# Kernel tuning notes

Hardware: AMD Instinct MI355X
Metric: run time of the kernel (lower is better)

## Reference

```python
import jax, jax.numpy as jnp
import numpy as np

N = 50000   # nodes
E = 800000  # edges (before self-loops)


def _gcn_conv(X, W, b, src, dst, dinv, n):
    # PyG GCNConv: out[i] = sum_j norm_ij * (X W)[j] + b, norm_ij = d_i^-1/2 d_j^-1/2
    h = X @ W                                   # [N, d_out]
    norm = dinv[src] * dinv[dst]                # [E+N]
    msg = h[src] * norm[:, None]                # gather + scale
    return jax.ops.segment_sum(msg, dst, num_segments=n) + b


def setup_inputs() -> dict:
    key = jax.random.key(0)
    k1, k2, k3, k4 = jax.random.split(key, 4)
    X = jax.random.normal(k1, (N, 128), dtype=jnp.float32)
    edge_index = jax.random.randint(k2, (2, E), 0, N, dtype=jnp.int64)
    W1 = jax.random.normal(k3, (128, 128), dtype=jnp.float32) * (1.0 / np.sqrt(128))
    b1 = jnp.zeros((128,), jnp.float32)
    W2 = jax.random.normal(k4, (128, 64), dtype=jnp.float32) * (1.0 / np.sqrt(128))
    b2 = jnp.zeros((64,), jnp.float32)
    return {"X": X, "edge_index": edge_index, "W1": W1, "b1": b1, "W2": W2, "b2": b2}


def reference(X, edge_index, W1, b1, W2, b2):
    n = X.shape[0]
    loops = jnp.arange(n, dtype=edge_index.dtype)
    src = jnp.concatenate([edge_index[0], loops])   # A + I
    dst = jnp.concatenate([edge_index[1], loops])
    deg = jax.ops.segment_sum(jnp.ones(src.shape[0], X.dtype), dst, num_segments=n)
    dinv = jnp.where(deg > 0, jax.lax.rsqrt(deg), 0.0)

    h = _gcn_conv(X, W1, b1, src, dst, dinv, n)                     # gcn1
    h = jax.nn.relu(_gcn_conv(h, W1, b1, src, dst, dinv, n))        # gcn1 again (as in source), relu
    # dropout: eval mode (identity)
    logits = _gcn_conv(h, W2, b2, src, dst, dinv, n)                # gcn2
    return jax.nn.log_softmax(logits, axis=1)
```

## Files before the change

kernel.cpp:

```cpp
#include <hip/hip_runtime.h>
#include <hip/hip_fp16.h>
#include <type_traits>

typedef _Float16 f16x8 __attribute__((ext_vector_type(8)));
typedef float    f32x4 __attribute__((ext_vector_type(4)));

__device__ inline unsigned int pack2(float a, float b) {
    __half2 h = __floats2half2_rn(a, b);
    return *(unsigned int*)&h;
}
__device__ inline float2 unpack2(unsigned int u) {
    __half2 h = *(__half2*)&u;
    return __half22float2(h);
}

#define MAXB 8192


__global__ void zero_kernel(int* __restrict__ p, int len) {
    int i = blockIdx.x * blockDim.x + threadIdx.x;
    if (i < len) p[i] = 0;
}

__global__ __launch_bounds__(256) void bucket_scatter_kernel(
    const int* __restrict__ src, const int* __restrict__ dst, int E, int nbuck,
    int* __restrict__ bcursor, unsigned int* __restrict__ staging) {
    __shared__ int hist[256];
    __shared__ int base[256];
    const int t = threadIdx.x;
    const int chunk = (E + gridDim.x - 1) / gridDim.x;
    const int e0 = blockIdx.x * chunk;
    const int e1 = min(E, e0 + chunk);
    for (int i = t; i < nbuck; i += 256) hist[i] = 0;
    __syncthreads();
    for (int e = e0 + t; e < e1; e += 256)
        atomicAdd(&hist[((unsigned)dst[e]) >> 8], 1);
    __syncthreads();
    for (int i = t; i < nbuck; i += 256) {
        int c = hist[i];
        base[i] = (c > 0) ? atomicAdd(&bcursor[i], c) : 0;
        hist[i] = 0;
    }
    __syncthreads();
    for (int e = e0 + t; e < e1; e += 256) {
        int d = dst[e];
        int b = ((unsigned)d) >> 8;
        int off = atomicAdd(&hist[b], 1);
        staging[(size_t)b * MAXB + base[b] + off] =
            (unsigned)src[e] | ((unsigned)(d & 255) << 16);
    }
}

__global__ __launch_bounds__(256) void bucket_hist_kernel(
    const unsigned int* __restrict__ staging, const int* __restrict__ bcursor,
    int n, int* __restrict__ counts) {
    __shared__ int hist[256];
    const int b = blockIdx.x, t = threadIdx.x;
    hist[t] = 0;
    __syncthreads();
    const int cnt = bcursor[b];
    const unsigned int* rec = staging + (size_t)b * MAXB;
    for (int i = t; i < cnt; i += 256) atomicAdd(&hist[(rec[i] >> 16) & 255], 1);
    __syncthreads();
    int node = (b << 8) + t;
    if (node < n) counts[node] = hist[t];
}

__global__ void dinv_kernel(const int* __restrict__ counts, float* __restrict__ dinv, int n) {
    int i = blockIdx.x * blockDim.x + threadIdx.x;
    if (i < n) dinv[i] = rsqrtf(1.0f + (float)counts[i]);
}


__global__ __launch_bounds__(256) void block_sum_kernel(const int* __restrict__ counts, int n,
                                                        int* __restrict__ blocksums) {
    __shared__ int s[256];
    int t = threadIdx.x;
    int i = blockIdx.x * 256 + t;
    s[t] = (i < n) ? counts[i] : 0;
    __syncthreads();
#pragma unroll
    for (int off = 128; off >= 1; off >>= 1) {
        if (t < off) s[t] += s[t + off];
        __syncthreads();
    }
    if (t == 0) blocksums[blockIdx.x] = s[0];
}

__global__ __launch_bounds__(256) void scan_blocksums_kernel(int* __restrict__ blocksums, int nb) {
    __shared__ int s[256];
    int t = threadIdx.x;
    int v = (t < nb) ? blocksums[t] : 0;
    s[t] = v;
    __syncthreads();
    for (int off = 1; off < 256; off <<= 1) {
        int u = (t >= off) ? s[t - off] : 0;
        __syncthreads();
        s[t] += u;
        __syncthreads();
    }
    if (t < nb) blocksums[t] = s[t] - v;
}

__global__ __launch_bounds__(256) void scan_write_kernel(const int* __restrict__ counts,
                                                         const int* __restrict__ blockoff, int n,
                                                         int* __restrict__ rowptr) {
    __shared__ int s[256];
    int t = threadIdx.x;
    int i = blockIdx.x * 256 + t;
    int v = (i < n) ? counts[i] : 0;
    s[t] = v;
    __syncthreads();
    for (int off = 1; off < 256; off <<= 1) {
        int u = (t >= off) ? s[t - off] : 0;
        __syncthreads();
        s[t] += u;
        __syncthreads();
    }
    int excl = blockoff[blockIdx.x] + s[t] - v;
    if (i < n) {
        rowptr[i] = excl;
        if (i == n - 1) rowptr[n] = excl + v;
    }
}

__global__ __launch_bounds__(256) void bucket_place_kernel(
    const unsigned int* __restrict__ staging, const int* __restrict__ bcursor,
    const int* __restrict__ rowptr, const float* __restrict__ dinv, int n,
    unsigned int* __restrict__ edges) {
    __shared__ int lcur[256];
    const int b = blockIdx.x, t = threadIdx.x;
    int node = (b << 8) + t;
    lcur[t] = rowptr[min(node, n)];
    __syncthreads();
    const int cnt = bcursor[b];
    const unsigned int* rec = staging + (size_t)b * MAXB;
    for (int i = t; i < cnt; i += 256) {
        unsigned r = rec[i];
        int dl = (r >> 16) & 255;
        int s  = r & 0xffff;
        int p  = atomicAdd(&lcur[dl], 1);
        __half hw = __float2half_rn(dinv[s] * dinv[(b << 8) + dl]);
        unsigned short ws = *(unsigned short*)&hw;
        edges[p] = (unsigned)s | ((unsigned)ws << 16);
    }
}

template <int DOUT, typename TIN>
__global__ __launch_bounds__(256) void gemm_mfma(const TIN* __restrict__ A,
                                                 const float* __restrict__ W,
                                                 __half* __restrict__ C, int n) {
    constexpr int NF = DOUT / 16;
    __shared__ __align__(16) unsigned char wlds[DOUT * 256];

    const int t = threadIdx.x;
    for (int p = t; p < 64 * DOUT; p += 256) {
        int nn = p % DOUT;
        int k  = (p / DOUT) * 2;
        float w0 = W[(size_t)k * DOUT + nn];
        float w1 = W[(size_t)(k + 1) * DOUT + nn];
        int byte = (nn * 256 + k * 2) ^ ((nn & 7) << 4);
        *(unsigned int*)(wlds + byte) = pack2(w0, w1);
    }
    __syncthreads();

    const int w  = t >> 6;
    const int l  = t & 63;
    const int m  = (blockIdx.x * 4 + w) * 16 + (l & 15);
    const int kq = l >> 4;
    const bool valid = (m < n);

    f32x4 acc[NF];
#pragma unroll
    for (int i = 0; i < NF; ++i) acc[i] = (f32x4){0.f, 0.f, 0.f, 0.f};

#pragma unroll
    for (int ks = 0; ks < 4; ++ks) {
        const int k0 = ks * 32 + kq * 8;
        f16x8 af = {0, 0, 0, 0, 0, 0, 0, 0};
        if (valid) {
            if constexpr (std::is_same<TIN, float>::value) {
                const float4 x0 = *(const float4*)&A[(size_t)m * 128 + k0];
                const float4 x1 = *(const float4*)&A[(size_t)m * 128 + k0 + 4];
                af[0] = (_Float16)x0.x; af[1] = (_Float16)x0.y;
                af[2] = (_Float16)x0.z; af[3] = (_Float16)x0.w;
                af[4] = (_Float16)x1.x; af[5] = (_Float16)x1.y;
                af[6] = (_Float16)x1.z; af[7] = (_Float16)x1.w;
            } else {
                af = *(const f16x8*)&A[(size_t)m * 128 + k0];
            }
        }
#pragma unroll
        for (int nf = 0; nf < NF; ++nf) {
            int nn = nf * 16 + (l & 15);
            int byte = (nn * 256 + k0 * 2) ^ ((nn & 7) << 4);
            f16x8 bf = *(const f16x8*)(wlds + byte);
            acc[nf] = __builtin_amdgcn_mfma_f32_16x16x32_f16(bf, af, acc[nf], 0, 0, 0);
        }
    }

    if (valid) {
#pragma unroll
        for (int nf = 0; nf < NF; ++nf) {
            uint2 o;
            o.x = pack2(acc[nf][0], acc[nf][1]);
            o.y = pack2(acc[nf][2], acc[nf][3]);
            *(uint2*)&C[(size_t)m * DOUT + nf * 16 + kq * 4] = o;
        }
    }
}

template <int DOUT, bool RELU, bool LSM, typename TOUT>
__global__ __launch_bounds__(256) void agg_kernel(const __half* __restrict__ H,
                                                  const int* __restrict__ rowptr,
                                                  const unsigned int* __restrict__ edges,
                                                  const float* __restrict__ dinv,
                                                  const float* __restrict__ bias,
                                                  TOUT* __restrict__ out, int n) {
    constexpr int LPR = DOUT / 8;
    constexpr int RPB = 256 / LPR;
    const int row  = blockIdx.x * RPB + threadIdx.x / LPR;
    const int lane = threadIdx.x % LPR;
    if (row >= n) return;

    const uint4* Hv = (const uint4*)H;

    float a[8];
    {
        const float4 b0 = ((const float4*)bias)[lane * 2];
        const float4 b1 = ((const float4*)bias)[lane * 2 + 1];
        const float di = dinv[row];
        const float sw = di * di;
        uint4 h = Hv[(size_t)row * LPR + lane];
        float2 f;
        f = unpack2(h.x); a[0] = b0.x + f.x * sw; a[1] = b0.y + f.y * sw;
        f = unpack2(h.y); a[2] = b0.z + f.x * sw; a[3] = b0.w + f.y * sw;
        f = unpack2(h.z); a[4] = b1.x + f.x * sw; a[5] = b1.y + f.y * sw;
        f = unpack2(h.w); a[6] = b1.z + f.x * sw; a[7] = b1.w + f.y * sw;
    }

    int j  = rowptr[row];
    const int je = rowptr[row + 1];
    for (; j + 1 < je; j += 2) {
        unsigned int e0 = edges[j], e1 = edges[j + 1];
        unsigned short u0 = (unsigned short)(e0 >> 16), u1 = (unsigned short)(e1 >> 16);
        float w0 = __half2float(*(__half*)&u0);
        float w1 = __half2float(*(__half*)&u1);
        uint4 h0 = Hv[(size_t)(e0 & 0xffffu) * LPR + lane];
        uint4 h1 = Hv[(size_t)(e1 & 0xffffu) * LPR + lane];
        float2 f;
        f = unpack2(h0.x); a[0] += w0 * f.x; a[1] += w0 * f.y;
        f = unpack2(h0.y); a[2] += w0 * f.x; a[3] += w0 * f.y;
        f = unpack2(h0.z); a[4] += w0 * f.x; a[5] += w0 * f.y;
        f = unpack2(h0.w); a[6] += w0 * f.x; a[7] += w0 * f.y;
        f = unpack2(h1.x); a[0] += w1 * f.x; a[1] += w1 * f.y;
        f = unpack2(h1.y); a[2] += w1 * f.x; a[3] += w1 * f.y;
        f = unpack2(h1.z); a[4] += w1 * f.x; a[5] += w1 * f.y;
        f = unpack2(h1.w); a[6] += w1 * f.x; a[7] += w1 * f.y;
    }
    if (j < je) {
        unsigned int e0 = edges[j];
        unsigned short u0 = (unsigned short)(e0 >> 16);
        float w0 = __half2float(*(__half*)&u0);
        uint4 h0 = Hv[(size_t)(e0 & 0xffffu) * LPR + lane];
        float2 f;
        f = unpack2(h0.x); a[0] += w0 * f.x; a[1] += w0 * f.y;
        f = unpack2(h0.y); a[2] += w0 * f.x; a[3] += w0 * f.y;
        f = unpack2(h0.z); a[4] += w0 * f.x; a[5] += w0 * f.y;
        f = unpack2(h0.w); a[6] += w0 * f.x; a[7] += w0 * f.y;
    }

    if (RELU) {
#pragma unroll
        for (int i = 0; i < 8; ++i) a[i] = fmaxf(a[i], 0.f);
    }

    if constexpr (LSM) {
        float m8 = a[0];
#pragma unroll
        for (int i = 1; i < 8; ++i) m8 = fmaxf(m8, a[i]);
#pragma unroll
        for (int off = 1; off < LPR; off <<= 1) m8 = fmaxf(m8, __shfl_xor(m8, off, LPR));
        float s = 0.f;
#pragma unroll
        for (int i = 0; i < 8; ++i) s += expf(a[i] - m8);
#pragma unroll
        for (int off = 1; off < LPR; off <<= 1) s += __shfl_xor(s, off, LPR);
        float ls = m8 + logf(s);
        float* op = (float*)out + (size_t)row * DOUT + lane * 8;
        *(float4*)op       = make_float4(a[0] - ls, a[1] - ls, a[2] - ls, a[3] - ls);
        *(float4*)(op + 4) = make_float4(a[4] - ls, a[5] - ls, a[6] - ls, a[7] - ls);
    } else {
        uint4 o;
        o.x = pack2(a[0], a[1]);
        o.y = pack2(a[2], a[3]);
        o.z = pack2(a[4], a[5]);
        o.w = pack2(a[6], a[7]);
        *(uint4*)&((__half*)out)[(size_t)row * DOUT + lane * 8] = o;
    }
}


extern "C" void kernel_launch(void* const* d_in, const int* in_sizes, int n_in,
                              void* d_out, int out_size, void* d_ws, size_t ws_size,
                              hipStream_t stream) {
    const float* X  = (const float*)d_in[0];
    const int*   ei = (const int*)d_in[1];
    const float* W1 = (const float*)d_in[2];
    const float* b1 = (const float*)d_in[3];
    const float* W2 = (const float*)d_in[4];
    const float* b2 = (const float*)d_in[5];

    const int n = in_sizes[0] / 128;
    const int E = in_sizes[1] / 2;
    const int* src = ei;
    const int* dst = ei + E;
    const int nbuck = (n + 255) >> 8;

    char* ws = (char*)d_ws;
    size_t off = 0;
    auto alloc = [&](size_t bytes) -> void* {
        void* p = ws + off;
        off = (off + bytes + 255) & ~(size_t)255;
        return p;
    };
    float*        dinv    = (float*)alloc((size_t)n * 4);
    int*          counts  = (int*)  alloc((size_t)n * 4);
    int*          rowptr  = (int*)  alloc((size_t)(n + 1) * 4);
    int*          bcursor = (int*)  alloc((size_t)nbuck * 4);
    int*          bsums   = (int*)  alloc(256 * 4);
    unsigned int* staging = (unsigned int*)alloc((size_t)nbuck * MAXB * 4);
    unsigned int* edges   = (unsigned int*)alloc((size_t)E * 4);
    __half*       P       = (__half*)alloc((size_t)n * 128 * 2);
    __half*       Q       = (__half*)alloc((size_t)n * 128 * 2);

    const int nb = (n + 255) / 256;

    zero_kernel<<<1, 256, 0, stream>>>(bcursor, nbuck);
    bucket_scatter_kernel<<<392, 256, 0, stream>>>(src, dst, E, nbuck, bcursor, staging);
    bucket_hist_kernel<<<nbuck, 256, 0, stream>>>(staging, bcursor, n, counts);
    block_sum_kernel<<<nb, 256, 0, stream>>>(counts, n, bsums);
    scan_blocksums_kernel<<<1, 256, 0, stream>>>(bsums, nb);
    scan_write_kernel<<<nb, 256, 0, stream>>>(counts, bsums, n, rowptr);
    dinv_kernel<<<(n + 255) / 256, 256, 0, stream>>>(counts, dinv, n);
    bucket_place_kernel<<<nbuck, 256, 0, stream>>>(staging, bcursor, rowptr, dinv, n, edges);

    const int gb = (n + 63) / 64;

    gemm_mfma<128, float><<<gb, 256, 0, stream>>>(X, W1, P, n);
    agg_kernel<128, false, false, __half><<<(n + 15) / 16, 256, 0, stream>>>(
        P, rowptr, edges, dinv, b1, Q, n);

    gemm_mfma<128, __half><<<gb, 256, 0, stream>>>(Q, W1, P, n);
    agg_kernel<128, true, false, __half><<<(n + 15) / 16, 256, 0, stream>>>(
        P, rowptr, edges, dinv, b1, Q, n);

    gemm_mfma<64, __half><<<gb, 256, 0, stream>>>(Q, W2, P, n);
    agg_kernel<64, false, true, float><<<(n + 31) / 32, 256, 0, stream>>>(
        P, rowptr, edges, dinv, b2, (float*)d_out, n);
}
```

Before: 182.4 us.

## Fold GCN normalization into GEMM epilogue, compact edges, split rows across a wavefront

Source-side dinv scaling now happens in the GEMM epilogue and destination-side scaling in the aggregation epilogue, so edges store only a 16-bit source index instead of a packed index plus fp16 weight. Aggregation gives each row a full 64-lane wavefront, with sub-groups taking strided edges and combining results through xor shuffles. This replaces the old layout of many rows per block with a few lanes each. The CSR build drops the count-scan and dinv kernels by scanning the bucket cursors directly and computing dinv in the histogram kernel. The trade-offs are shuffle reduction overhead and idle lanes on low-degree rows.

```diff
diff --git a/kernel.cpp b/kernel.cpp
--- a/kernel.cpp
+++ b/kernel.cpp
@@ -53,7 +53,7 @@
 
 __global__ __launch_bounds__(256) void bucket_hist_kernel(
     const unsigned int* __restrict__ staging, const int* __restrict__ bcursor,
-    int n, int* __restrict__ counts) {
+    int n, int* __restrict__ counts, float* __restrict__ dinv) {
     __shared__ int hist[256];
     const int b = blockIdx.x, t = threadIdx.x;
     hist[t] = 0;
@@ -63,34 +63,18 @@
     for (int i = t; i < cnt; i += 256) atomicAdd(&hist[(rec[i] >> 16) & 255], 1);
     __syncthreads();
     int node = (b << 8) + t;
-    if (node < n) counts[node] = hist[t];
-}
-
-__global__ void dinv_kernel(const int* __restrict__ counts, float* __restrict__ dinv, int n) {
-    int i = blockIdx.x * blockDim.x + threadIdx.x;
-    if (i < n) dinv[i] = rsqrtf(1.0f + (float)counts[i]);
-}
-
-
-__global__ __launch_bounds__(256) void block_sum_kernel(const int* __restrict__ counts, int n,
-                                                        int* __restrict__ blocksums) {
+    if (node < n) {
+        int c = hist[t];
+        counts[node] = c;
+        dinv[node]   = rsqrtf(1.0f + (float)c);
+    }
+}
+
+__global__ __launch_bounds__(256) void scan_bexcl_kernel(const int* __restrict__ bcursor,
+                                                         int* __restrict__ bexcl, int nb) {
     __shared__ int s[256];
     int t = threadIdx.x;
-    int i = blockIdx.x * 256 + t;
-    s[t] = (i < n) ? counts[i] : 0;
-    __syncthreads();
-#pragma unroll
-    for (int off = 128; off >= 1; off >>= 1) {
-        if (t < off) s[t] += s[t + off];
-        __syncthreads();
-    }
-    if (t == 0) blocksums[blockIdx.x] = s[0];
-}
-
-__global__ __launch_bounds__(256) void scan_blocksums_kernel(int* __restrict__ blocksums, int nb) {
-    __shared__ int s[256];
-    int t = threadIdx.x;
-    int v = (t < nb) ? blocksums[t] : 0;
+    int v = (t < nb) ? bcursor[t] : 0;
     s[t] = v;
     __syncthreads();
     for (int off = 1; off < 256; off <<= 1) {
@@ -99,7 +83,7 @@
         s[t] += u;
         __syncthreads();
     }
-    if (t < nb) blocksums[t] = s[t] - v;
+    if (t < nb) bexcl[t] = s[t] - v;
 }
 
 __global__ __launch_bounds__(256) void scan_write_kernel(const int* __restrict__ counts,
@@ -126,8 +110,7 @@
 
 __global__ __launch_bounds__(256) void bucket_place_kernel(
     const unsigned int* __restrict__ staging, const int* __restrict__ bcursor,
-    const int* __restrict__ rowptr, const float* __restrict__ dinv, int n,
-    unsigned int* __restrict__ edges) {
+    const int* __restrict__ rowptr, int n, unsigned short* __restrict__ edges) {
     __shared__ int lcur[256];
     const int b = blockIdx.x, t = threadIdx.x;
     int node = (b << 8) + t;
@@ -138,17 +121,15 @@
     for (int i = t; i < cnt; i += 256) {
         unsigned r = rec[i];
         int dl = (r >> 16) & 255;
-        int s  = r & 0xffff;
         int p  = atomicAdd(&lcur[dl], 1);
-        __half hw = __float2half_rn(dinv[s] * dinv[(b << 8) + dl]);
-        unsigned short ws = *(unsigned short*)&hw;
-        edges[p] = (unsigned)s | ((unsigned)ws << 16);
+        edges[p] = (unsigned short)(r & 0xffffu);
     }
 }
 
 template <int DOUT, typename TIN>
 __global__ __launch_bounds__(256) void gemm_mfma(const TIN* __restrict__ A,
                                                  const float* __restrict__ W,
+                                                 const float* __restrict__ dinv,
                                                  __half* __restrict__ C, int n) {
     constexpr int NF = DOUT / 16;
     __shared__ __align__(16) unsigned char wlds[DOUT * 256];
@@ -200,11 +181,12 @@
     }
 
     if (valid) {
+        const float di = dinv[m];
 #pragma unroll
         for (int nf = 0; nf < NF; ++nf) {
             uint2 o;
-            o.x = pack2(acc[nf][0], acc[nf][1]);
-            o.y = pack2(acc[nf][2], acc[nf][3]);
+            o.x = pack2(di * acc[nf][0], di * acc[nf][1]);
+            o.y = pack2(di * acc[nf][2], di * acc[nf][3]);
             *(uint2*)&C[(size_t)m * DOUT + nf * 16 + kq * 4] = o;
         }
     }
@@ -213,62 +195,57 @@
 template <int DOUT, bool RELU, bool LSM, typename TOUT>
 __global__ __launch_bounds__(256) void agg_kernel(const __half* __restrict__ H,
                                                   const int* __restrict__ rowptr,
-                                                  const unsigned int* __restrict__ edges,
+                                                  const unsigned short* __restrict__ edges,
                                                   const float* __restrict__ dinv,
                                                   const float* __restrict__ bias,
                                                   TOUT* __restrict__ out, int n) {
     constexpr int LPR = DOUT / 8;
-    constexpr int RPB = 256 / LPR;
-    const int row  = blockIdx.x * RPB + threadIdx.x / LPR;
-    const int lane = threadIdx.x % LPR;
+    constexpr int EPW = 64 / LPR;
+    const int t    = threadIdx.x;
+    const int row  = blockIdx.x * 4 + (t >> 6);
     if (row >= n) return;
+    const int lane = t & 63;
+    const int sub  = lane / LPR;
+    const int fl   = lane % LPR;
 
     const uint4* Hv = (const uint4*)H;
 
-    float a[8];
-    {
-        const float4 b0 = ((const float4*)bias)[lane * 2];
-        const float4 b1 = ((const float4*)bias)[lane * 2 + 1];
-        const float di = dinv[row];
-        const float sw = di * di;
-        uint4 h = Hv[(size_t)row * LPR + lane];
+    float a[8] = {0.f, 0.f, 0.f, 0.f, 0.f, 0.f, 0.f, 0.f};
+    auto accum = [&](uint4 h) {
         float2 f;
-        f = unpack2(h.x); a[0] = b0.x + f.x * sw; a[1] = b0.y + f.y * sw;
-        f = unpack2(h.y); a[2] = b0.z + f.x * sw; a[3] = b0.w + f.y * sw;
-        f = unpack2(h.z); a[4] = b1.x + f.x * sw; a[5] = b1.y + f.y * sw;
-        f = unpack2(h.w); a[6] = b1.z + f.x * sw; a[7] = b1.w + f.y * sw;
-    }
-
-    int j  = rowptr[row];
+        f = unpack2(h.x); a[0] += f.x; a[1] += f.y;
+        f = unpack2(h.y); a[2] += f.x; a[3] += f.y;
+        f = unpack2(h.z); a[4] += f.x; a[5] += f.y;
+        f = unpack2(h.w); a[6] += f.x; a[7] += f.y;
+    };
+
+    if (sub == 0) accum(Hv[(size_t)row * LPR + fl]);
+
+    int j        = rowptr[row] + sub;
     const int je = rowptr[row + 1];
-    for (; j + 1 < je; j += 2) {
-        unsigned int e0 = edges[j], e1 = edges[j + 1];
-        unsigned short u0 = (unsigned short)(e0 >> 16), u1 = (unsigned short)(e1 >> 16);
-        float w0 = __half2float(*(__half*)&u0);
-        float w1 = __half2float(*(__half*)&u1);
-        uint4 h0 = Hv[(size_t)(e0 & 0xffffu) * LPR + lane];
-        uint4 h1 = Hv[(size_t)(e1 & 0xffffu) * LPR + lane];
-        float2 f;
-        f = unpack2(h0.x); a[0] += w0 * f.x; a[1] += w0 * f.y;
-        f = unpack2(h0.y); a[2] += w0 * f.x; a[3] += w0 * f.y;
-        f = unpack2(h0.z); a[4] += w0 * f.x; a[5] += w0 * f.y;
-        f = unpack2(h0.w); a[6] += w0 * f.x; a[7] += w0 * f.y;
-        f = unpack2(h1.x); a[0] += w1 * f.x; a[1] += w1 * f.y;
-        f = unpack2(h1.y); a[2] += w1 * f.x; a[3] += w1 * f.y;
-        f = unpack2(h1.z); a[4] += w1 * f.x; a[5] += w1 * f.y;
-        f = unpack2(h1.w); a[6] += w1 * f.x; a[7] += w1 * f.y;
-    }
-    if (j < je) {
-        unsigned int e0 = edges[j];
-        unsigned short u0 = (unsigned short)(e0 >> 16);
-        float w0 = __half2float(*(__half*)&u0);
-        uint4 h0 = Hv[(size_t)(e0 & 0xffffu) * LPR + lane];
-        float2 f;
-        f = unpack2(h0.x); a[0] += w0 * f.x; a[1] += w0 * f.y;
-        f = unpack2(h0.y); a[2] += w0 * f.x; a[3] += w0 * f.y;
-        f = unpack2(h0.z); a[4] += w0 * f.x; a[5] += w0 * f.y;
-        f = unpack2(h0.w); a[6] += w0 * f.x; a[7] += w0 * f.y;
-    }
+    for (; j + EPW < je; j += 2 * EPW) {
+        int s0 = edges[j];
+        int s1 = edges[j + EPW];
+        uint4 h0 = Hv[(size_t)s0 * LPR + fl];
+        uint4 h1 = Hv[(size_t)s1 * LPR + fl];
+        accum(h0);
+        accum(h1);
+    }
+    if (j < je) accum(Hv[(size_t)edges[j] * LPR + fl]);
+
+#pragma unroll
+    for (int off = LPR; off < 64; off <<= 1) {
+#pragma unroll
+        for (int i = 0; i < 8; ++i) a[i] += __shfl_xor(a[i], off, 64);
+    }
+
+    const float di = dinv[row];
+    const float4 b0 = ((const float4*)bias)[fl * 2];
+    const float4 b1 = ((const float4*)bias)[fl * 2 + 1];
+    a[0] = b0.x + di * a[0]; a[1] = b0.y + di * a[1];
+    a[2] = b0.z + di * a[2]; a[3] = b0.w + di * a[3];
+    a[4] = b1.x + di * a[4]; a[5] = b1.y + di * a[5];
+    a[6] = b1.z + di * a[6]; a[7] = b1.w + di * a[7];
 
     if (RELU) {
 #pragma unroll
@@ -287,16 +264,20 @@
 #pragma unroll
         for (int off = 1; off < LPR; off <<= 1) s += __shfl_xor(s, off, LPR);
         float ls = m8 + logf(s);
-        float* op = (float*)out + (size_t)row * DOUT + lane * 8;
-        *(float4*)op       = make_float4(a[0] - ls, a[1] - ls, a[2] - ls, a[3] - ls);
-        *(float4*)(op + 4) = make_float4(a[4] - ls, a[5] - ls, a[6] - ls, a[7] - ls);
+        if (sub == 0) {
+            float* op = (float*)out + (size_t)row * DOUT + fl * 8;
+            *(float4*)op       = make_float4(a[0] - ls, a[1] - ls, a[2] - ls, a[3] - ls);
+            *(float4*)(op + 4) = make_float4(a[4] - ls, a[5] - ls, a[6] - ls, a[7] - ls);
+        }
     } else {
-        uint4 o;
-        o.x = pack2(a[0], a[1]);
-        o.y = pack2(a[2], a[3]);
-        o.z = pack2(a[4], a[5]);
-        o.w = pack2(a[6], a[7]);
-        *(uint4*)&((__half*)out)[(size_t)row * DOUT + lane * 8] = o;
+        if (sub == 0) {
+            uint4 o;
+            o.x = pack2(a[0], a[1]);
+            o.y = pack2(a[2], a[3]);
+            o.z = pack2(a[4], a[5]);
+            o.w = pack2(a[6], a[7]);
+            *(uint4*)&((__half*)out)[(size_t)row * DOUT + fl * 8] = o;
+        }
     }
 }
 
@@ -324,38 +305,37 @@
         off = (off + bytes + 255) & ~(size_t)255;
         return p;
     };
-    float*        dinv    = (float*)alloc((size_t)n * 4);
-    int*          counts  = (int*)  alloc((size_t)n * 4);
-    int*          rowptr  = (int*)  alloc((size_t)(n + 1) * 4);
-    int*          bcursor = (int*)  alloc((size_t)nbuck * 4);
-    int*          bsums   = (int*)  alloc(256 * 4);
-    unsigned int* staging = (unsigned int*)alloc((size_t)nbuck * MAXB * 4);
-    unsigned int* edges   = (unsigned int*)alloc((size_t)E * 4);
-    __half*       P       = (__half*)alloc((size_t)n * 128 * 2);
-    __half*       Q       = (__half*)alloc((size_t)n * 128 * 2);
+    float*          dinv    = (float*)alloc((size_t)n * 4);
+    int*            counts  = (int*)  alloc((size_t)n * 4);
+    int*            rowptr  = (int*)  alloc((size_t)(n + 1) * 4);
+    int*            bcursor = (int*)  alloc((size_t)nbuck * 4);
+    int*            bexcl   = (int*)  alloc((size_t)nbuck * 4);
+    unsigned int*   staging = (unsigned int*)alloc((size_t)nbuck * MAXB * 4);
+    unsigned short* edges   = (unsigned short*)alloc((size_t)E * 2);
+    __half*         P       = (__half*)alloc((size_t)n * 128 * 2);
+    __half*         Q       = (__half*)alloc((size_t)n * 128 * 2);
 
     const int nb = (n + 255) / 256;
 
     zero_kernel<<<1, 256, 0, stream>>>(bcursor, nbuck);
     bucket_scatter_kernel<<<392, 256, 0, stream>>>(src, dst, E, nbuck, bcursor, staging);
-    bucket_hist_kernel<<<nbuck, 256, 0, stream>>>(staging, bcursor, n, counts);
-    block_sum_kernel<<<nb, 256, 0, stream>>>(counts, n, bsums);
-    scan_blocksums_kernel<<<1, 256, 0, stream>>>(bsums, nb);
-    scan_write_kernel<<<nb, 256, 0, stream>>>(counts, bsums, n, rowptr);
-    dinv_kernel<<<(n + 255) / 256, 256, 0, stream>>>(counts, dinv, n);
-    bucket_place_kernel<<<nbuck, 256, 0, stream>>>(staging, bcursor, rowptr, dinv, n, edges);
+    bucket_hist_kernel<<<nbuck, 256, 0, stream>>>(staging, bcursor, n, counts, dinv);
+    scan_bexcl_kernel<<<1, 256, 0, stream>>>(bcursor, bexcl, nbuck);
+    scan_write_kernel<<<nb, 256, 0, stream>>>(counts, bexcl, n, rowptr);
+    bucket_place_kernel<<<nbuck, 256, 0, stream>>>(staging, bcursor, rowptr, n, edges);
 
     const int gb = (n + 63) / 64;
-
-    gemm_mfma<128, float><<<gb, 256, 0, stream>>>(X, W1, P, n);
-    agg_kernel<128, false, false, __half><<<(n + 15) / 16, 256, 0, stream>>>(
+    const int ab = (n + 3) / 4;
+
+    gemm_mfma<128, float><<<gb, 256, 0, stream>>>(X, W1, dinv, P, n);
+    agg_kernel<128, false, false, __half><<<ab, 256, 0, stream>>>(
         P, rowptr, edges, dinv, b1, Q, n);
 
-    gemm_mfma<128, __half><<<gb, 256, 0, stream>>>(Q, W1, P, n);
-    agg_kernel<128, true, false, __half><<<(n + 15) / 16, 256, 0, stream>>>(
+    gemm_mfma<128, __half><<<gb, 256, 0, stream>>>(Q, W1, dinv, P, n);
+    agg_kernel<128, true, false, __half><<<ab, 256, 0, stream>>>(
         P, rowptr, edges, dinv, b1, Q, n);
 
-    gemm_mfma<64, __half><<<gb, 256, 0, stream>>>(Q, W2, P, n);
-    agg_kernel<64, false, true, float><<<(n + 31) / 32, 256, 0, stream>>>(
+    gemm_mfma<64, __half><<<gb, 256, 0, stream>>>(Q, W2, dinv, P, n);
+    agg_kernel<64, false, true, float><<<ab, 256, 0, stream>>>(
         P, rowptr, edges, dinv, b2, (float*)d_out, n);
 }
```

Result: slower. 193.7 us (+6.2%).
